# Kernel tuning notes

Measured on AMD Instinct MI355X. Metric: run time of the kernel, lower is better.

## Reference

```python
import jax, jax.numpy as jnp
import numpy as np

DIM = 2048
N_HEADS = 32
N_KV_HEADS = 8
HEAD_DIM = DIM // N_HEADS  # 64
N_REP = N_HEADS // N_KV_HEADS  # 4
SEQ = 2048
BSZ = 1


def _rope(x, cos, sin):
    # x: [b, s, h, hd]; cos/sin: [s, hd//2]
    x2 = x.reshape(*x.shape[:-1], HEAD_DIM // 2, 2)
    xe, xo = x2[..., 0], x2[..., 1]
    c = cos[None, :, None, :]
    s = sin[None, :, None, :]
    oe = xe * c - xo * s
    oo = xe * s + xo * c
    return jnp.stack([oe, oo], axis=-1).reshape(x.shape)


def setup_inputs() -> dict:
    key = jax.random.key(0)
    ks = jax.random.split(key, 6)
    x = jax.random.normal(ks[0], (BSZ, SEQ, DIM), dtype=jnp.float32)
    # llama-style rotary freqs
    inv = 1.0 / (10000.0 ** (np.arange(0, HEAD_DIM, 2, dtype=np.float32) / HEAD_DIM))
    t = np.arange(SEQ, dtype=np.float32)
    ang = np.outer(t, inv)  # [s, hd//2]
    freqs_cos = jnp.asarray(np.cos(ang))
    freqs_sin = jnp.asarray(np.sin(ang))
    # additive causal mask
    mask = jnp.where(jnp.tril(jnp.ones((SEQ, SEQ), bool)), 0.0, -jnp.inf).astype(jnp.float32)
    sc = 1.0 / np.sqrt(DIM)
    wq = jax.random.normal(ks[1], (DIM, N_HEADS * HEAD_DIM), jnp.float32) * sc
    wk = jax.random.normal(ks[2], (DIM, N_KV_HEADS * HEAD_DIM), jnp.float32) * sc
    wv = jax.random.normal(ks[3], (DIM, N_KV_HEADS * HEAD_DIM), jnp.float32) * sc
    wo = jax.random.normal(ks[4], (N_HEADS * HEAD_DIM, DIM), jnp.float32) * sc
    return {"x": x, "freqs_cos": freqs_cos, "freqs_sin": freqs_sin, "mask": mask,
            "wq": wq, "wk": wk, "wv": wv, "wo": wo}


def reference(x, freqs_cos, freqs_sin, mask, wq, wk, wv, wo):
    b, s, _ = x.shape
    xq = (x @ wq).reshape(b, s, N_HEADS, HEAD_DIM)
    xk = (x @ wk).reshape(b, s, N_KV_HEADS, HEAD_DIM)
    xv = (x @ wv).reshape(b, s, N_KV_HEADS, HEAD_DIM)
    xq = _rope(xq, freqs_cos, freqs_sin)
    xk = _rope(xk, freqs_cos, freqs_sin)
    # repeat_kv: expand kv heads by n_rep
    xk = jnp.repeat(xk, N_REP, axis=2)  # [b, s, H, hd]
    xv = jnp.repeat(xv, N_REP, axis=2)
    scores = jnp.einsum('bqhd,bkhd->bhqk', xq, xk) / np.sqrt(HEAD_DIM)
    scores = scores + mask[None, None, :, :]
    probs = jax.nn.softmax(scores.astype(jnp.float32), axis=-1).astype(xq.dtype)
    out = jnp.einsum('bhqk,bkhd->bqhd', probs, xv).reshape(b, s, N_HEADS * HEAD_DIM)
    return out @ wo
```

## Files before the change

kernel.cpp:

```cpp
#include <hip/hip_runtime.h>
#include <hip/hip_bf16.h>

#define SEQ  2048
#define DIM  2048
#define NQK  3072
#define NH   32
#define NKV  8
#define HD   64

typedef __attribute__((ext_vector_type(8))) short s8v;
typedef __attribute__((ext_vector_type(4))) short s4v;
typedef __attribute__((ext_vector_type(4))) float f32x4;

__device__ __forceinline__ short f2bf_bits(float f) {
    __hip_bfloat16 b = __float2bfloat16(f);
    short s; __builtin_memcpy(&s, &b, 2); return s;
}
__device__ __forceinline__ float bfbits2f(short s) {
    __hip_bfloat16 b; __builtin_memcpy(&b, &s, 2);
    return __bfloat162float(b);
}
__device__ __forceinline__ f32x4 mfma16(s8v a, s8v b, f32x4 c) {
    return __builtin_amdgcn_mfma_f32_16x16x32_bf16(a, b, c, 0, 0, 0);
}
__device__ __forceinline__ void load16_to_lds(const void* g, void* l) {
    __builtin_amdgcn_global_load_lds(
        (const __attribute__((address_space(1))) void*)g,
        (__attribute__((address_space(3))) void*)l, 16, 0, 0);
}
__device__ __forceinline__ float fexp2(float x) {
    float y; asm("v_exp_f32 %0, %1" : "=v"(y) : "v"(x)); return y;
}

__global__ void cvt_f32_bf16(const float* __restrict__ src, short* __restrict__ dst) {
    int i = (blockIdx.x * 256 + threadIdx.x) * 4;
    float4 v = *(const float4*)(src + i);
    s4v o;
    o.x = f2bf_bits(v.x); o.y = f2bf_bits(v.y);
    o.z = f2bf_bits(v.z); o.w = f2bf_bits(v.w);
    *(s4v*)(dst + i) = o;
}

__global__ void transpose_cvt(const float* __restrict__ src, short* __restrict__ dst, int Cs) {
    __shared__ float tile[32][33];
    int bx = blockIdx.x * 32, by = blockIdx.y * 32;
    int tx = threadIdx.x, ty = threadIdx.y;
    #pragma unroll
    for (int j = 0; j < 32; j += 8)
        tile[ty + j][tx] = src[(size_t)(by + ty + j) * Cs + bx + tx];
    __syncthreads();
    #pragma unroll
    for (int j = 0; j < 32; j += 8)
        dst[(size_t)(bx + ty + j) * 2048 + by + tx] = f2bf_bits(tile[tx][ty + j]);
}

__global__ __launch_bounds__(256, 3)
void gemm_bt(const short* __restrict__ A, const short* __restrict__ BT,
             short* __restrict__ P0, short* __restrict__ P1,
             int N, int K, int nx)
{
    __shared__ short As[128 * 64];
    __shared__ short Bs[128 * 64];
    const int nwg = gridDim.x;
    const int orig = blockIdx.x;
    const int wg = (orig & 7) * (nwg >> 3) + (orig >> 3);
    const int ks  = wg & 1;
    const int bxy = wg >> 1;
    const int bm = (bxy / nx) * 128, bn = (bxy % nx) * 128;

    const int lane = threadIdx.x & 63;
    const int wid  = threadIdx.x >> 6;
    const int r = lane & 15, g = lane >> 4;
    const int wm = (wid >> 1) * 64, wn = (wid & 1) * 64;

    f32x4 acc[4][4];
    #pragma unroll
    for (int i = 0; i < 4; ++i)
        #pragma unroll
        for (int j = 0; j < 4; ++j) acc[i][j] = (f32x4){0.f, 0.f, 0.f, 0.f};

    const int srow = wid * 32 + (lane >> 3);
    const int scol = (lane & 7) * 8;
    const int kbeg = ks * (K >> 1), kend = kbeg + (K >> 1);

    for (int k0 = kbeg; k0 < kend; k0 += 64) {
        #pragma unroll
        for (int s2 = 0; s2 < 4; ++s2) {
            int row = srow + s2 * 8;
            int seg = wid * 4 + s2;
            load16_to_lds(A  + (size_t)(bm + row) * K + k0 + scol, As + seg * 512);
            load16_to_lds(BT + (size_t)(bn + row) * K + k0 + scol, Bs + seg * 512);
        }
        __syncthreads();
        #pragma unroll
        for (int kk = 0; kk < 64; kk += 32) {
            s8v a[4], b[4];
            #pragma unroll
            for (int t = 0; t < 4; ++t)
                a[t] = *(const s8v*)&As[(wm + t * 16 + r) * 64 + kk + g * 8];
            #pragma unroll
            for (int t = 0; t < 4; ++t)
                b[t] = *(const s8v*)&Bs[(wn + t * 16 + r) * 64 + kk + g * 8];
            __builtin_amdgcn_s_setprio(1);
            #pragma unroll
            for (int i = 0; i < 4; ++i)
                #pragma unroll
                for (int j = 0; j < 4; ++j)
                    acc[i][j] = mfma16(a[i], b[j], acc[i][j]);
            __builtin_amdgcn_s_setprio(0);
        }
        __syncthreads();
    }

    short* P = ks ? P1 : P0;
    #pragma unroll
    for (int i = 0; i < 4; ++i)
        #pragma unroll
        for (int j = 0; j < 4; ++j)
            #pragma unroll
            for (int q = 0; q < 4; ++q) {
                int row = bm + wm + i * 16 + g * 4 + q;
                int col = bn + wn + j * 16 + r;
                P[(size_t)row * N + col] = f2bf_bits(acc[i][j][q]);
            }
}

__global__ void rope_add(const short* __restrict__ P0, const short* __restrict__ P1,
                         short* __restrict__ qkv,
                         const float* __restrict__ fc, const float* __restrict__ fs) {
    int idx = blockIdx.x * 256 + threadIdx.x;
    int row = idx / 320;
    int col = (idx - row * 320) * 8;
    s8v a = *(const s8v*)(P0 + (size_t)row * NQK + col);
    s8v b = *(const s8v*)(P1 + (size_t)row * NQK + col);
    int p0 = (col & 63) >> 1;
    s8v o;
    #pragma unroll
    for (int k = 0; k < 4; ++k) {
        float xe = bfbits2f(a[2 * k])     + bfbits2f(b[2 * k]);
        float xo = bfbits2f(a[2 * k + 1]) + bfbits2f(b[2 * k + 1]);
        float c  = fc[row * 32 + p0 + k];
        float sn = fs[row * 32 + p0 + k];
        o[2 * k]     = f2bf_bits(xe * c - xo * sn);
        o[2 * k + 1] = f2bf_bits(xe * sn + xo * c);
    }
    *(s8v*)(qkv + (size_t)row * NQK + col) = o;
}

__global__ void vT_add(const short* __restrict__ P0, const short* __restrict__ P1,
                       short* __restrict__ vT) {
    __shared__ float tile[32][33];
    int bx = blockIdx.x * 32;
    int by = blockIdx.y * 32;
    int tx = threadIdx.x, ty = threadIdx.y;
    #pragma unroll
    for (int j = 0; j < 32; j += 8) {
        size_t off = (size_t)(by + ty + j) * NQK + 2560 + bx + tx;
        tile[ty + j][tx] = bfbits2f(P0[off]) + bfbits2f(P1[off]);
    }
    __syncthreads();
    #pragma unroll
    for (int j = 0; j < 32; j += 8)
        vT[(size_t)(bx + ty + j) * 2048 + by + tx] = f2bf_bits(tile[tx][ty + j]);
}

__global__ void add_out(const short* __restrict__ R0, const short* __restrict__ R1,
                        float* __restrict__ out) {
    int i = (blockIdx.x * 256 + threadIdx.x) * 8;
    s8v a = *(const s8v*)(R0 + i);
    s8v b = *(const s8v*)(R1 + i);
    float4 o0, o1;
    o0.x = bfbits2f(a[0]) + bfbits2f(b[0]);
    o0.y = bfbits2f(a[1]) + bfbits2f(b[1]);
    o0.z = bfbits2f(a[2]) + bfbits2f(b[2]);
    o0.w = bfbits2f(a[3]) + bfbits2f(b[3]);
    o1.x = bfbits2f(a[4]) + bfbits2f(b[4]);
    o1.y = bfbits2f(a[5]) + bfbits2f(b[5]);
    o1.z = bfbits2f(a[6]) + bfbits2f(b[6]);
    o1.w = bfbits2f(a[7]) + bfbits2f(b[7]);
    *(float4*)(out + i)     = o0;
    *(float4*)(out + i + 4) = o1;
}

#define SCL 0.18033688f
__global__ __launch_bounds__(256, 4)
void flash_attn(const short* __restrict__ qkv, const short* __restrict__ vT,
                short* __restrict__ O) {
    const int h  = blockIdx.x;
    const int qi = (int)gridDim.y - 1 - (int)blockIdx.y;
    const int qb = qi * 64;
    const int kh = h >> 2;
    const int lane = threadIdx.x & 63;
    const int wid  = threadIdx.x >> 6;
    const int r = lane & 15, g = lane >> 4;

    __shared__ short Ks[64][72];
    __shared__ short Vt[64][72];
    __shared__ short Pl[4][16][72];

    s8v qf0, qf1;
    {
        const short* qrow = qkv + (size_t)(qb + wid * 16 + r) * NQK + h * 64;
        qf0 = *(const s8v*)(qrow + g * 8);
        qf1 = *(const s8v*)(qrow + 32 + g * 8);
    }

    float m[4], l[4];
    f32x4 o[4];
    #pragma unroll
    for (int q = 0; q < 4; ++q) { m[q] = -1e30f; l[q] = 0.f; }
    #pragma unroll
    for (int t = 0; t < 4; ++t) o[t] = (f32x4){0.f, 0.f, 0.f, 0.f};

    const int tr = threadIdx.x >> 2;
    const int tc = (threadIdx.x & 3) * 16;

    const int nkt = qi + 1;
    for (int kt = 0; kt < nkt; ++kt) {
        {
            const short* kg = qkv + (size_t)(kt * 64 + tr) * NQK + 2048 + kh * 64 + tc;
            *(s8v*)&Ks[tr][tc]     = *(const s8v*)kg;
            *(s8v*)&Ks[tr][tc + 8] = *(const s8v*)(kg + 8);
            const short* vg = vT + (size_t)(kh * 64 + tr) * 2048 + kt * 64 + tc;
            *(s8v*)&Vt[tr][tc]     = *(const s8v*)vg;
            *(s8v*)&Vt[tr][tc + 8] = *(const s8v*)(vg + 8);
        }
        __syncthreads();

        f32x4 s[4];
        __builtin_amdgcn_s_setprio(1);
        #pragma unroll
        for (int t = 0; t < 4; ++t) {
            s8v kb0 = *(const s8v*)&Ks[t * 16 + r][g * 8];
            s8v kb1 = *(const s8v*)&Ks[t * 16 + r][32 + g * 8];
            f32x4 z = (f32x4){0.f, 0.f, 0.f, 0.f};
            z = mfma16(qf0, kb0, z);
            z = mfma16(qf1, kb1, z);
            s[t] = z;
        }
        __builtin_amdgcn_s_setprio(0);

        const bool diag = (kt == nkt - 1);
        #pragma unroll
        for (int t = 0; t < 4; ++t)
            #pragma unroll
            for (int q = 0; q < 4; ++q) {
                float v = s[t][q] * SCL;
                if (diag) {
                    int qrow = qb + wid * 16 + g * 4 + q;
                    int kpos = kt * 64 + t * 16 + r;
                    if (kpos > qrow) v = -1e30f;
                }
                s[t][q] = v;
            }

        float pm[4];
        #pragma unroll
        for (int q = 0; q < 4; ++q) {
            float v = fmaxf(fmaxf(s[0][q], s[1][q]), fmaxf(s[2][q], s[3][q]));
            #pragma unroll
            for (int off = 1; off < 16; off <<= 1) v = fmaxf(v, __shfl_xor(v, off, 64));
            pm[q] = v;
        }
        bool need = (pm[0] > m[0] + 8.f) || (pm[1] > m[1] + 8.f) ||
                    (pm[2] > m[2] + 8.f) || (pm[3] > m[3] + 8.f);
        if (__any(need)) {
            #pragma unroll
            for (int q = 0; q < 4; ++q) {
                float mn = fmaxf(m[q], pm[q]);
                float al = fexp2(m[q] - mn);
                m[q] = mn;
                l[q] *= al;
                #pragma unroll
                for (int t = 0; t < 4; ++t) o[t][q] *= al;
            }
        }
        #pragma unroll
        for (int t = 0; t < 4; ++t)
            #pragma unroll
            for (int q = 0; q < 4; ++q)
                s[t][q] = fexp2(s[t][q] - m[q]);
        #pragma unroll
        for (int q = 0; q < 4; ++q) {
            float v = (s[0][q] + s[1][q]) + (s[2][q] + s[3][q]);
            #pragma unroll
            for (int off = 1; off < 16; off <<= 1) v += __shfl_xor(v, off, 64);
            l[q] += v;
        }
        #pragma unroll
        for (int t = 0; t < 4; ++t)
            #pragma unroll
            for (int q = 0; q < 4; ++q)
                Pl[wid][g * 4 + q][t * 16 + r] = f2bf_bits(s[t][q]);
        asm volatile("s_waitcnt lgkmcnt(0)" ::: "memory");

        s8v pa0 = *(const s8v*)&Pl[wid][r][g * 8];
        s8v pa1 = *(const s8v*)&Pl[wid][r][32 + g * 8];
        __builtin_amdgcn_s_setprio(1);
        #pragma unroll
        for (int t = 0; t < 4; ++t) {
            s8v vb0 = *(const s8v*)&Vt[t * 16 + r][g * 8];
            s8v vb1 = *(const s8v*)&Vt[t * 16 + r][32 + g * 8];
            o[t] = mfma16(pa0, vb0, o[t]);
            o[t] = mfma16(pa1, vb1, o[t]);
        }
        __builtin_amdgcn_s_setprio(0);
        __syncthreads();
    }

    float rl[4];
    #pragma unroll
    for (int q = 0; q < 4; ++q) rl[q] = __builtin_amdgcn_rcpf(l[q]);
    #pragma unroll
    for (int t = 0; t < 4; ++t)
        #pragma unroll
        for (int q = 0; q < 4; ++q) {
            float val = o[t][q] * rl[q];
            O[(size_t)(qb + wid * 16 + g * 4 + q) * 2048 + h * 64 + t * 16 + r] = f2bf_bits(val);
        }
}

extern "C" void kernel_launch(void* const* d_in, const int* in_sizes, int n_in,
                              void* d_out, int out_size, void* d_ws, size_t ws_size,
                              hipStream_t stream)
{
    const float* x  = (const float*)d_in[0];
    const float* fc = (const float*)d_in[1];
    const float* fs = (const float*)d_in[2];
    const float* wq = (const float*)d_in[4];
    const float* wk = (const float*)d_in[5];
    const float* wv = (const float*)d_in[6];
    const float* wo = (const float*)d_in[7];
    float* out = (float*)d_out;

    char* ws = (char*)d_ws;
    short* xb    = (short*)(ws);
    short* wqkvT = (short*)(ws + 8  * 1024 * 1024);
    short* woT   = (short*)(ws + 20 * 1024 * 1024);
    short* qkv   = (short*)(ws + 28 * 1024 * 1024);
    short* vT    = (short*)(ws + 40 * 1024 * 1024);
    short* attnO = (short*)(ws + 42 * 1024 * 1024);
    short* P0    = (short*)(ws + 50 * 1024 * 1024);
    short* P1    = (short*)(ws + 63 * 1024 * 1024);

    dim3 tb(32, 8);
    cvt_f32_bf16<<<4096, 256, 0, stream>>>(x, xb);
    transpose_cvt<<<dim3(64, 64), tb, 0, stream>>>(wq, wqkvT, 2048);
    transpose_cvt<<<dim3(16, 64), tb, 0, stream>>>(wk, wqkvT + 2048 * 2048, 512);
    transpose_cvt<<<dim3(16, 64), tb, 0, stream>>>(wv, wqkvT + 2560 * 2048, 512);
    transpose_cvt<<<dim3(64, 64), tb, 0, stream>>>(wo, woT, 2048);

    gemm_bt<<<768, 256, 0, stream>>>(xb, wqkvT, P0, P1, 3072, 2048, 24);
    rope_add<<<2560, 256, 0, stream>>>(P0, P1, qkv, fc, fs);
    vT_add<<<dim3(16, 64), tb, 0, stream>>>(P0, P1, vT);

    flash_attn<<<dim3(32, 32), 256, 0, stream>>>(qkv, vT, attnO);

    gemm_bt<<<512, 256, 0, stream>>>(attnO, woT, P0, P1, 2048, 2048, 16);
    add_out<<<2048, 256, 0, stream>>>(P0, P1, out);
}
```

Measured before the change: 272.3 us.

## Fold softmax scale into RoPE, transpose score MFMA, 3-way split-K output GEMM

The softmax scale (log2e/sqrt(d)) is folded into the Q rows during the RoPE pass, so the attention kernel no longer multiplies every score. Attention now computes K·Q so each lane holds one query row. That replaces the per-row 16-lane shuffle reductions for max and sum with two cross-group shuffles, and the P tile is stored with an XOR swizzle as packed 4-element writes. The output projection is split 3 ways along K into 768 workgroups to fill more CUs, with the third partial written into the now-free qkv buffer and a three-input add kernel. The split adds extra partial-sum traffic and a K slice that is not a multiple of 128.

```diff
diff --git a/kernel.cpp b/kernel.cpp
--- a/kernel.cpp
+++ b/kernel.cpp
@@ -7,6 +7,7 @@
 #define NH   32
 #define NKV  8
 #define HD   64
+#define SCL  0.18033688f
 
 typedef __attribute__((ext_vector_type(8))) short s8v;
 typedef __attribute__((ext_vector_type(4))) short s4v;
@@ -54,9 +55,10 @@
         dst[(size_t)(bx + ty + j) * 2048 + by + tx] = f2bf_bits(tile[tx][ty + j]);
 }
 
+template<int S>
 __global__ __launch_bounds__(256, 3)
 void gemm_bt(const short* __restrict__ A, const short* __restrict__ BT,
-             short* __restrict__ P0, short* __restrict__ P1,
+             short* __restrict__ P0, short* __restrict__ P1, short* __restrict__ P2,
              int N, int K, int nx)
 {
     __shared__ short As[128 * 64];
@@ -64,9 +66,13 @@
     const int nwg = gridDim.x;
     const int orig = blockIdx.x;
     const int wg = (orig & 7) * (nwg >> 3) + (orig >> 3);
-    const int ks  = wg & 1;
-    const int bxy = wg >> 1;
+    const int per = nwg / S;
+    const int ks  = wg / per;
+    const int bxy = wg - ks * per;
     const int bm = (bxy / nx) * 128, bn = (bxy % nx) * 128;
+    const int kslice = ((K / S) + 63) & ~63;
+    const int kbeg = ks * kslice;
+    const int kend = (kbeg + kslice < K) ? (kbeg + kslice) : K;
 
     const int lane = threadIdx.x & 63;
     const int wid  = threadIdx.x >> 6;
@@ -81,7 +87,6 @@
 
     const int srow = wid * 32 + (lane >> 3);
     const int scol = (lane & 7) * 8;
-    const int kbeg = ks * (K >> 1), kend = kbeg + (K >> 1);
 
     for (int k0 = kbeg; k0 < kend; k0 += 64) {
         #pragma unroll
@@ -112,7 +117,7 @@
         __syncthreads();
     }
 
-    short* P = ks ? P1 : P0;
+    short* P = (ks == 0) ? P0 : ((ks == 1) ? P1 : P2);
     #pragma unroll
     for (int i = 0; i < 4; ++i)
         #pragma unroll
@@ -134,6 +139,7 @@
     s8v a = *(const s8v*)(P0 + (size_t)row * NQK + col);
     s8v b = *(const s8v*)(P1 + (size_t)row * NQK + col);
     int p0 = (col & 63) >> 1;
+    float scl = (col < 2048) ? SCL : 1.0f;
     s8v o;
     #pragma unroll
     for (int k = 0; k < 4; ++k) {
@@ -141,8 +147,8 @@
         float xo = bfbits2f(a[2 * k + 1]) + bfbits2f(b[2 * k + 1]);
         float c  = fc[row * 32 + p0 + k];
         float sn = fs[row * 32 + p0 + k];
-        o[2 * k]     = f2bf_bits(xe * c - xo * sn);
-        o[2 * k + 1] = f2bf_bits(xe * sn + xo * c);
+        o[2 * k]     = f2bf_bits((xe * c - xo * sn) * scl);
+        o[2 * k + 1] = f2bf_bits((xe * sn + xo * c) * scl);
     }
     *(s8v*)(qkv + (size_t)row * NQK + col) = o;
 }
@@ -164,25 +170,23 @@
         vT[(size_t)(bx + ty + j) * 2048 + by + tx] = f2bf_bits(tile[tx][ty + j]);
 }
 
-__global__ void add_out(const short* __restrict__ R0, const short* __restrict__ R1,
-                        float* __restrict__ out) {
+__global__ void add_out3(const short* __restrict__ R0, const short* __restrict__ R1,
+                         const short* __restrict__ R2, float* __restrict__ out) {
     int i = (blockIdx.x * 256 + threadIdx.x) * 8;
     s8v a = *(const s8v*)(R0 + i);
     s8v b = *(const s8v*)(R1 + i);
-    float4 o0, o1;
-    o0.x = bfbits2f(a[0]) + bfbits2f(b[0]);
-    o0.y = bfbits2f(a[1]) + bfbits2f(b[1]);
-    o0.z = bfbits2f(a[2]) + bfbits2f(b[2]);
-    o0.w = bfbits2f(a[3]) + bfbits2f(b[3]);
-    o1.x = bfbits2f(a[4]) + bfbits2f(b[4]);
-    o1.y = bfbits2f(a[5]) + bfbits2f(b[5]);
-    o1.z = bfbits2f(a[6]) + bfbits2f(b[6]);
-    o1.w = bfbits2f(a[7]) + bfbits2f(b[7]);
-    *(float4*)(out + i)     = o0;
-    *(float4*)(out + i + 4) = o1;
-}
-
-#define SCL 0.18033688f
+    s8v c = *(const s8v*)(R2 + i);
+    #pragma unroll
+    for (int k = 0; k < 8; k += 4) {
+        float4 o;
+        o.x = bfbits2f(a[k])     + bfbits2f(b[k])     + bfbits2f(c[k]);
+        o.y = bfbits2f(a[k + 1]) + bfbits2f(b[k + 1]) + bfbits2f(c[k + 1]);
+        o.z = bfbits2f(a[k + 2]) + bfbits2f(b[k + 2]) + bfbits2f(c[k + 2]);
+        o.w = bfbits2f(a[k + 3]) + bfbits2f(b[k + 3]) + bfbits2f(c[k + 3]);
+        *(float4*)(out + i + k) = o;
+    }
+}
+
 __global__ __launch_bounds__(256, 4)
 void flash_attn(const short* __restrict__ qkv, const short* __restrict__ vT,
                 short* __restrict__ O) {
@@ -205,15 +209,14 @@
         qf1 = *(const s8v*)(qrow + 32 + g * 8);
     }
 
-    float m[4], l[4];
+    float mrow = -1e30f, lrow = 0.f;
     f32x4 o[4];
-    #pragma unroll
-    for (int q = 0; q < 4; ++q) { m[q] = -1e30f; l[q] = 0.f; }
     #pragma unroll
     for (int t = 0; t < 4; ++t) o[t] = (f32x4){0.f, 0.f, 0.f, 0.f};
 
     const int tr = threadIdx.x >> 2;
     const int tc = (threadIdx.x & 3) * 16;
+    const int xm = (r & 3) << 3;
 
     const int nkt = qi + 1;
     for (int kt = 0; kt < nkt; ++kt) {
@@ -231,71 +234,69 @@
         __builtin_amdgcn_s_setprio(1);
         #pragma unroll
         for (int t = 0; t < 4; ++t) {
-            s8v kb0 = *(const s8v*)&Ks[t * 16 + r][g * 8];
-            s8v kb1 = *(const s8v*)&Ks[t * 16 + r][32 + g * 8];
+            s8v ka0 = *(const s8v*)&Ks[t * 16 + r][g * 8];
+            s8v ka1 = *(const s8v*)&Ks[t * 16 + r][32 + g * 8];
             f32x4 z = (f32x4){0.f, 0.f, 0.f, 0.f};
-            z = mfma16(qf0, kb0, z);
-            z = mfma16(qf1, kb1, z);
+            z = mfma16(ka0, qf0, z);
+            z = mfma16(ka1, qf1, z);
             s[t] = z;
         }
         __builtin_amdgcn_s_setprio(0);
 
-        const bool diag = (kt == nkt - 1);
+        if (kt == nkt - 1) {
+            const int qrow = qb + wid * 16 + r;
+            #pragma unroll
+            for (int t = 0; t < 4; ++t)
+                #pragma unroll
+                for (int q = 0; q < 4; ++q)
+                    if (kt * 64 + t * 16 + g * 4 + q > qrow) s[t][q] = -1e30f;
+        }
+
+        float pm = fmaxf(fmaxf(fmaxf(s[0][0], s[0][1]), fmaxf(s[0][2], s[0][3])),
+                         fmaxf(fmaxf(s[1][0], s[1][1]), fmaxf(s[1][2], s[1][3])));
+        pm = fmaxf(pm, fmaxf(fmaxf(fmaxf(s[2][0], s[2][1]), fmaxf(s[2][2], s[2][3])),
+                             fmaxf(fmaxf(s[3][0], s[3][1]), fmaxf(s[3][2], s[3][3]))));
+        pm = fmaxf(pm, __shfl_xor(pm, 16, 64));
+        pm = fmaxf(pm, __shfl_xor(pm, 32, 64));
+
+        if (__any(pm > mrow + 8.f)) {
+            float mn = fmaxf(mrow, pm);
+            float al = fexp2(mrow - mn);
+            mrow = mn;
+            lrow *= al;
+            float alq[4];
+            #pragma unroll
+            for (int q = 0; q < 4; ++q) alq[q] = __shfl(al, g * 4 + q, 64);
+            #pragma unroll
+            for (int t = 0; t < 4; ++t)
+                #pragma unroll
+                for (int q = 0; q < 4; ++q) o[t][q] *= alq[q];
+        }
+
+        float rs = 0.f;
         #pragma unroll
         for (int t = 0; t < 4; ++t)
             #pragma unroll
             for (int q = 0; q < 4; ++q) {
-                float v = s[t][q] * SCL;
-                if (diag) {
-                    int qrow = qb + wid * 16 + g * 4 + q;
-                    int kpos = kt * 64 + t * 16 + r;
-                    if (kpos > qrow) v = -1e30f;
-                }
-                s[t][q] = v;
+                float p = fexp2(s[t][q] - mrow);
+                s[t][q] = p;
+                rs += p;
             }
-
-        float pm[4];
-        #pragma unroll
-        for (int q = 0; q < 4; ++q) {
-            float v = fmaxf(fmaxf(s[0][q], s[1][q]), fmaxf(s[2][q], s[3][q]));
-            #pragma unroll
-            for (int off = 1; off < 16; off <<= 1) v = fmaxf(v, __shfl_xor(v, off, 64));
-            pm[q] = v;
-        }
-        bool need = (pm[0] > m[0] + 8.f) || (pm[1] > m[1] + 8.f) ||
-                    (pm[2] > m[2] + 8.f) || (pm[3] > m[3] + 8.f);
-        if (__any(need)) {
-            #pragma unroll
-            for (int q = 0; q < 4; ++q) {
-                float mn = fmaxf(m[q], pm[q]);
-                float al = fexp2(m[q] - mn);
-                m[q] = mn;
-                l[q] *= al;
-                #pragma unroll
-                for (int t = 0; t < 4; ++t) o[t][q] *= al;
-            }
-        }
-        #pragma unroll
-        for (int t = 0; t < 4; ++t)
-            #pragma unroll
-            for (int q = 0; q < 4; ++q)
-                s[t][q] = fexp2(s[t][q] - m[q]);
-        #pragma unroll
-        for (int q = 0; q < 4; ++q) {
-            float v = (s[0][q] + s[1][q]) + (s[2][q] + s[3][q]);
-            #pragma unroll
-            for (int off = 1; off < 16; off <<= 1) v += __shfl_xor(v, off, 64);
-            l[q] += v;
-        }
-        #pragma unroll
-        for (int t = 0; t < 4; ++t)
-            #pragma unroll
-            for (int q = 0; q < 4; ++q)
-                Pl[wid][g * 4 + q][t * 16 + r] = f2bf_bits(s[t][q]);
+        rs += __shfl_xor(rs, 16, 64);
+        rs += __shfl_xor(rs, 32, 64);
+        lrow += rs;
+
+        #pragma unroll
+        for (int t = 0; t < 4; ++t) {
+            s4v pk;
+            #pragma unroll
+            for (int q = 0; q < 4; ++q) pk[q] = f2bf_bits(s[t][q]);
+            *(s4v*)&Pl[wid][r][(t * 16 + g * 4) ^ xm] = pk;
+        }
         asm volatile("s_waitcnt lgkmcnt(0)" ::: "memory");
 
-        s8v pa0 = *(const s8v*)&Pl[wid][r][g * 8];
-        s8v pa1 = *(const s8v*)&Pl[wid][r][32 + g * 8];
+        s8v pa0 = *(const s8v*)&Pl[wid][r][(g * 8) ^ xm];
+        s8v pa1 = *(const s8v*)&Pl[wid][r][32 + ((g * 8) ^ xm)];
         __builtin_amdgcn_s_setprio(1);
         #pragma unroll
         for (int t = 0; t < 4; ++t) {
@@ -308,16 +309,16 @@
         __syncthreads();
     }
 
-    float rl[4];
-    #pragma unroll
-    for (int q = 0; q < 4; ++q) rl[q] = __builtin_amdgcn_rcpf(l[q]);
+    float rl = __builtin_amdgcn_rcpf(lrow);
+    float rlq[4];
+    #pragma unroll
+    for (int q = 0; q < 4; ++q) rlq[q] = __shfl(rl, g * 4 + q, 64);
     #pragma unroll
     for (int t = 0; t < 4; ++t)
         #pragma unroll
-        for (int q = 0; q < 4; ++q) {
-            float val = o[t][q] * rl[q];
-            O[(size_t)(qb + wid * 16 + g * 4 + q) * 2048 + h * 64 + t * 16 + r] = f2bf_bits(val);
-        }
+        for (int q = 0; q < 4; ++q)
+            O[(size_t)(qb + wid * 16 + g * 4 + q) * 2048 + h * 64 + t * 16 + r] =
+                f2bf_bits(o[t][q] * rlq[q]);
 }
 
 extern "C" void kernel_launch(void* const* d_in, const int* in_sizes, int n_in,
@@ -342,6 +343,7 @@
     short* attnO = (short*)(ws + 42 * 1024 * 1024);
     short* P0    = (short*)(ws + 50 * 1024 * 1024);
     short* P1    = (short*)(ws + 63 * 1024 * 1024);
+    short* P2o   = qkv;
 
     dim3 tb(32, 8);
     cvt_f32_bf16<<<4096, 256, 0, stream>>>(x, xb);
@@ -350,12 +352,12 @@
     transpose_cvt<<<dim3(16, 64), tb, 0, stream>>>(wv, wqkvT + 2560 * 2048, 512);
     transpose_cvt<<<dim3(64, 64), tb, 0, stream>>>(wo, woT, 2048);
 
-    gemm_bt<<<768, 256, 0, stream>>>(xb, wqkvT, P0, P1, 3072, 2048, 24);
+    gemm_bt<2><<<768, 256, 0, stream>>>(xb, wqkvT, P0, P1, nullptr, 3072, 2048, 24);
     rope_add<<<2560, 256, 0, stream>>>(P0, P1, qkv, fc, fs);
     vT_add<<<dim3(16, 64), tb, 0, stream>>>(P0, P1, vT);
 
     flash_attn<<<dim3(32, 32), 256, 0, stream>>>(qkv, vT, attnO);
 
-    gemm_bt<<<512, 256, 0, stream>>>(attnO, woT, P0, P1, 2048, 2048, 16);
-    add_out<<<2048, 256, 0, stream>>>(P0, P1, out);
-}
+    gemm_bt<3><<<768, 256, 0, stream>>>(attnO, woT, P0, P1, P2o, 2048, 2048, 16);
+    add_out3<<<2048, 256, 0, stream>>>(P0, P1, P2o, out);
+}
```

Result: faster. 252.7 us (-7.2%).
